# Kernel tuning notes

Hardware: AMD Instinct MI355X
Metric: run time of the kernel (lower is better)

The kernel has to match this reference:

```python
import jax, jax.numpy as jnp
import numpy as np

N, E, R, H = 20000, 320000, 8, 4
KG, CC = 128, 4
IN, HID, OUT = 256, 256, 256  # in_channels = KG + 128 (GCN out)
HO1, HO2 = HID // H, OUT // H  # per-head out channels
SLOPE_ACT = 0.01   # nn.LeakyReLU default
SLOPE_ATT = 0.2    # RGATConv negative_slope default


def gcn_conv(x, W, b, src, dst):
    """PyG GCNConv: add self loops, symmetric norm, x@W, scatter-sum, +bias."""
    n = x.shape[0]
    loop = jnp.arange(n, dtype=src.dtype)
    s = jnp.concatenate([src, loop])
    d = jnp.concatenate([dst, loop])
    deg = jnp.zeros((n,), x.dtype).at[d].add(1.0)
    dis = jnp.where(deg > 0, jax.lax.rsqrt(jnp.maximum(deg, 1.0)), 0.0)
    norm = dis[s] * dis[d]                        # [E+N]
    h = x @ W                                     # [n, out]
    out = jax.ops.segment_sum(norm[:, None] * h[s], d, num_segments=n)
    return out + b


def rgat_conv(x, W, q, k, b, src, dst, edge_type, heads, oc):
    """PyG RGATConv (additive-self-attention, across-relation, dim=1, concat)."""
    n = x.shape[0]
    xw = jnp.einsum('ni,rio->rno', x, W)          # [R, n, heads*oc]
    out_i = xw[edge_type, dst]                    # [E, heads*oc]
    out_j = xw[edge_type, src]                    # [E, heads*oc]
    qi = out_i @ q                                # [E, heads]
    kj = out_j @ k                                # [E, heads]
    alpha = jax.nn.leaky_relu(qi + kj, SLOPE_ATT)
    # softmax over incoming edges per destination node (across-relation)
    amax = jax.ops.segment_max(alpha, dst, num_segments=n)[dst]
    ex = jnp.exp(alpha - amax)
    denom = jax.ops.segment_sum(ex, dst, num_segments=n)[dst]
    alpha = ex / denom                            # [E, heads]
    e = src.shape[0]
    msg = (alpha[:, :, None] * out_j.reshape(e, heads, oc)).reshape(e, heads * oc)
    out = jax.ops.segment_sum(msg, dst, num_segments=n) + b
    return out, alpha


def setup_inputs() -> dict:
    key = jax.random.key(0)
    ks = jax.random.split(key, 16)
    d = {}
    d['kg_emb'] = jax.random.normal(ks[0], (N, KG), jnp.float32)
    d['ccle0'] = jax.random.normal(ks[1], (N, CC), jnp.float32)
    d['gcn_w1'] = jax.random.normal(ks[2], (CC, 32), jnp.float32) / np.float32(np.sqrt(CC))
    d['gcn_b1'] = jnp.zeros((32,), jnp.float32)
    d['gcn_w2'] = jax.random.normal(ks[3], (32, 128), jnp.float32) / np.float32(np.sqrt(32))
    d['gcn_b2'] = jnp.zeros((128,), jnp.float32)
    d['rgat1_w'] = jax.random.normal(ks[4], (R, IN, HID), jnp.float32) / np.float32(np.sqrt(IN))
    d['rgat1_q'] = jax.random.normal(ks[5], (HID, H), jnp.float32) / np.float32(np.sqrt(HID))
    d['rgat1_k'] = jax.random.normal(ks[6], (HID, H), jnp.float32) / np.float32(np.sqrt(HID))
    d['rgat1_b'] = jnp.zeros((HID,), jnp.float32)
    d['rgat2_w'] = jax.random.normal(ks[7], (R, HID, OUT), jnp.float32) / np.float32(np.sqrt(HID))
    d['rgat2_q'] = jax.random.normal(ks[8], (OUT, H), jnp.float32) / np.float32(np.sqrt(OUT))
    d['rgat2_k'] = jax.random.normal(ks[9], (OUT, H), jnp.float32) / np.float32(np.sqrt(OUT))
    d['rgat2_b'] = jnp.zeros((OUT,), jnp.float32)
    d['lin_w'] = jax.random.normal(ks[10], (IN, OUT), jnp.float32) / np.float32(np.sqrt(IN))
    d['lin_b'] = jnp.zeros((OUT,), jnp.float32)
    d['edge_index'] = jax.random.randint(ks[11], (2, E), 0, N, jnp.int32)
    d['edge_type'] = jax.random.randint(ks[12], (E,), 0, R, jnp.int32)
    return d


def reference(kg_emb, ccle0, gcn_w1, gcn_b1, gcn_w2, gcn_b2,
              rgat1_w, rgat1_q, rgat1_k, rgat1_b,
              rgat2_w, rgat2_q, rgat2_k, rgat2_b,
              lin_w, lin_b, edge_index, edge_type):
    src, dst = edge_index[0], edge_index[1]
    # ccle_layer: GCN(4->32) -> LeakyReLU -> GCN(32->128)
    c = gcn_conv(ccle0, gcn_w1, gcn_b1, src, dst)
    c = jax.nn.leaky_relu(c, SLOPE_ACT)
    c = gcn_conv(c, gcn_w2, gcn_b2, src, dst)
    # node_id = arange(N): concat(kg_emb, ccle_out)
    x0 = jnp.concatenate([kg_emb, c], axis=1)     # [N, IN]
    h, a1 = rgat_conv(x0, rgat1_w, rgat1_q, rgat1_k, rgat1_b,
                      src, dst, edge_type, H, HO1)
    h = jax.nn.leaky_relu(h, SLOPE_ACT)           # dropout p=0 -> identity
    h, a2 = rgat_conv(h, rgat2_w, rgat2_q, rgat2_k, rgat2_b,
                      src, dst, edge_type, H, HO2)
    out = h + (x0 @ lin_w + lin_b)                # residual through self.lin
    return out, a1, a2
```

## Files before the change

kernel.cpp:

```cpp
#include <hip/hip_runtime.h>
#include <cstdint>

static constexpr int N = 20000;
static constexpr int E = 320000;
static constexpr int R = 8;
static constexpr int H = 4;
static constexpr int C = 256;

using short8 = __attribute__((ext_vector_type(8))) short;
using f32x4  = __attribute__((ext_vector_type(4))) float;
using us4    = __attribute__((ext_vector_type(4))) unsigned short;

__device__ __forceinline__ float lrelu(float x, float s) { return x >= 0.f ? x : s * x; }
__device__ __forceinline__ unsigned short f2bf(float f) {
    unsigned u = __float_as_uint(f);
    unsigned r = (u + 0x7FFFu + ((u >> 16) & 1u)) >> 16;
    return (unsigned short)r;
}
__device__ __forceinline__ float bf2f(unsigned short s) {
    return __uint_as_float(((unsigned)s) << 16);
}

__device__ __forceinline__ void gl2l16(const unsigned short* g, unsigned short* l) {
    __builtin_amdgcn_global_load_lds(
        (const __attribute__((address_space(1))) unsigned int*)g,
        (__attribute__((address_space(3))) unsigned int*)l, 16, 0, 0);
}

__global__ void k_zero_int(int* p, int n) {
    int i = blockIdx.x * blockDim.x + threadIdx.x;
    if (i < n) p[i] = 0;
}

__global__ void k_count(const int* __restrict__ ei, int* __restrict__ cnt) {
    int e = blockIdx.x * blockDim.x + threadIdx.x;
    if (e < E) atomicAdd(&cnt[ei[E + e]], 1);
}

__global__ __launch_bounds__(1024) void k_scan(const int* __restrict__ cnt,
                                               int* __restrict__ rowptr,
                                               int* __restrict__ cursor,
                                               float* __restrict__ dis) {
    __shared__ int part[1024];
    const int CH = (N + 1023) / 1024;
    int t = threadIdx.x;
    int base = t * CH;
    int sum = 0;
    for (int j = 0; j < CH; ++j) {
        int idx = base + j;
        if (idx < N) sum += cnt[idx];
    }
    part[t] = sum;
    __syncthreads();
    for (int off = 1; off < 1024; off <<= 1) {
        int v = 0;
        if (t >= off) v = part[t - off];
        __syncthreads();
        if (t >= off) part[t] += v;
        __syncthreads();
    }
    int run = part[t] - sum;
    for (int j = 0; j < CH; ++j) {
        int idx = base + j;
        if (idx < N) {
            int cv = cnt[idx];
            rowptr[idx] = run;
            cursor[idx] = run;
            dis[idx] = rsqrtf((float)cv + 1.0f);
            run += cv;
        }
    }
    if (t == 1023) rowptr[N] = part[1023];
}

__global__ void k_scatter(const int* __restrict__ ei, const int* __restrict__ et,
                          int* __restrict__ cursor, int* __restrict__ csr_se,
                          int* __restrict__ csr_eid) {
    int e = blockIdx.x * blockDim.x + threadIdx.x;
    if (e >= E) return;
    int d = ei[E + e];
    int pos = atomicAdd(&cursor[d], 1);
    csr_se[pos] = (et[e] << 16) | ei[e];
    csr_eid[pos] = e;
}

__global__ void k_h1(const float* __restrict__ x, const float* __restrict__ W,
                     float* __restrict__ h) {
    int idx = blockIdx.x * blockDim.x + threadIdx.x;
    if (idx >= N * 32) return;
    int n = idx >> 5, f = idx & 31;
    const float* xr = x + n * 4;
    float acc = 0.f;
#pragma unroll
    for (int c = 0; c < 4; ++c) acc += xr[c] * W[c * 32 + f];
    h[idx] = acc;
}

__global__ void k_agg32(const int* __restrict__ rowptr, const int* __restrict__ csr_se,
                        const float* __restrict__ dis, const float* __restrict__ h,
                        const float* __restrict__ b, float* __restrict__ c) {
    int idx = blockIdx.x * blockDim.x + threadIdx.x;
    if (idx >= N * 32) return;
    int d = idx >> 5, f = idx & 31;
    int beg = rowptr[d], end = rowptr[d + 1];
    float acc = 0.f;
    for (int i = beg; i < end; ++i) {
        int s = csr_se[i] & 0xFFFF;
        acc += dis[s] * h[s * 32 + f];
    }
    float dd = dis[d];
    c[idx] = dd * acc + dd * dd * h[idx] + b[f];
}

__global__ void k_h2kg(const float* __restrict__ c1, const float* __restrict__ W,
                       const float* __restrict__ kg, unsigned short* __restrict__ h,
                       float* __restrict__ x0, unsigned short* __restrict__ xb0) {
    int idx = blockIdx.x * blockDim.x + threadIdx.x;
    if (idx >= N * 128) return;
    int n = idx >> 7, f = idx & 127;
    const float* cr = c1 + n * 32;
    float acc = 0.f;
    for (int c = 0; c < 32; ++c) acc += lrelu(cr[c], 0.01f) * W[c * 128 + f];
    h[idx] = f2bf(acc);
    float v = kg[idx];
    x0[n * 256 + f] = v;
    xb0[n * 256 + f] = f2bf(v);
}

__global__ void k_agg128(const int* __restrict__ rowptr, const int* __restrict__ csr_se,
                         const float* __restrict__ dis,
                         const unsigned short* __restrict__ h,
                         const float* __restrict__ b, float* __restrict__ x0,
                         unsigned short* __restrict__ xb0) {
    int idx = blockIdx.x * blockDim.x + threadIdx.x;
    if (idx >= N * 128) return;
    int d = idx >> 7, f = idx & 127;
    int beg = rowptr[d], end = rowptr[d + 1];
    float acc = 0.f;
    int i = beg;
    for (; i + 2 <= end; i += 2) {
        int s0 = csr_se[i] & 0xFFFF;
        int s1 = csr_se[i + 1] & 0xFFFF;
        float d0 = dis[s0], d1 = dis[s1];
        float v0 = bf2f(h[s0 * 128 + f]), v1 = bf2f(h[s1 * 128 + f]);
        acc += d0 * v0 + d1 * v1;
    }
    if (i < end) {
        int s = csr_se[i] & 0xFFFF;
        acc += dis[s] * bf2f(h[s * 128 + f]);
    }
    float dd = dis[d];
    float v = dd * acc + dd * dd * bf2f(h[d * 128 + f]) + b[f];
    x0[d * 256 + 128 + f] = v;
    xb0[d * 256 + 128 + f] = f2bf(v);
}

__global__ __launch_bounds__(256) void k_wqkb(const float* __restrict__ W,
                                              const float* __restrict__ q,
                                              const float* __restrict__ kmat,
                                              unsigned short* __restrict__ wqkb) {
    int w = (blockIdx.x * blockDim.x + threadIdx.x) >> 6;
    int lane = threadIdx.x & 63;
    int r = w >> 8, i = w & 255;
    const float* wr = W + ((size_t)(r * 256 + i)) * 256;
    float4 a = *(const float4*)(wr + lane * 4);
    float aq0 = 0.f, aq1 = 0.f, aq2 = 0.f, aq3 = 0.f;
    float ak0 = 0.f, ak1 = 0.f, ak2 = 0.f, ak3 = 0.f;
    int o = lane * 4;
    const float av[4] = {a.x, a.y, a.z, a.w};
#pragma unroll
    for (int j = 0; j < 4; ++j) {
        float4 qv = *(const float4*)(q + (o + j) * 4);
        float4 kv = *(const float4*)(kmat + (o + j) * 4);
        aq0 += av[j] * qv.x; aq1 += av[j] * qv.y;
        aq2 += av[j] * qv.z; aq3 += av[j] * qv.w;
        ak0 += av[j] * kv.x; ak1 += av[j] * kv.y;
        ak2 += av[j] * kv.z; ak3 += av[j] * kv.w;
    }
#pragma unroll
    for (int d = 1; d < 64; d <<= 1) {
        aq0 += __shfl_xor(aq0, d); aq1 += __shfl_xor(aq1, d);
        aq2 += __shfl_xor(aq2, d); aq3 += __shfl_xor(aq3, d);
        ak0 += __shfl_xor(ak0, d); ak1 += __shfl_xor(ak1, d);
        ak2 += __shfl_xor(ak2, d); ak3 += __shfl_xor(ak3, d);
    }
    if (lane == 0) {
        int nq = r * 4, nk = 32 + r * 4;
        wqkb[(nq + 0) * 256 + i] = f2bf(aq0);
        wqkb[(nq + 1) * 256 + i] = f2bf(aq1);
        wqkb[(nq + 2) * 256 + i] = f2bf(aq2);
        wqkb[(nq + 3) * 256 + i] = f2bf(aq3);
        wqkb[(nk + 0) * 256 + i] = f2bf(ak0);
        wqkb[(nk + 1) * 256 + i] = f2bf(ak1);
        wqkb[(nk + 2) * 256 + i] = f2bf(ak2);
        wqkb[(nk + 3) * 256 + i] = f2bf(ak3);
    }
}

#define QP 264
__global__ __launch_bounds__(256) void k_qnkn_mfma(
    const unsigned short* __restrict__ xb, const unsigned short* __restrict__ wqkb,
    float* __restrict__ qn, float* __restrict__ kn)
{
    __shared__ unsigned short Ws[64 * QP];
    int t = threadIdx.x;
    {
        int r = t >> 2, off = (t & 3) * 64;
#pragma unroll
        for (int i = 0; i < 8; ++i)
            *(uint4*)(&Ws[r * QP + off + i * 8]) =
                *(const uint4*)(wqkb + r * 256 + off + i * 8);
    }
    __syncthreads();
    int wave = t >> 6, lane = t & 63;
    int lrow = lane & 15, kq = lane >> 4;
    int mw = blockIdx.x * 64 + wave * 16;
    int gm = mw + lrow;
    int gmc = gm < N ? gm : N - 1;

    f32x4 acc[4];
#pragma unroll
    for (int j = 0; j < 4; ++j) acc[j] = (f32x4){0.f, 0.f, 0.f, 0.f};

    for (int k0 = 0; k0 < 8; ++k0) {
        short8 af = *(const short8*)(xb + (size_t)gmc * 256 + k0 * 32 + kq * 8);
#pragma unroll
        for (int j = 0; j < 4; ++j) {
            short8 bf4 = *(const short8*)(&Ws[(j * 16 + lrow) * QP + k0 * 32 + kq * 8]);
            acc[j] = __builtin_amdgcn_mfma_f32_16x16x32_bf16(bf4, af, acc[j], 0, 0, 0);
        }
    }
    if (gm < N) {
#pragma unroll
        for (int j = 0; j < 4; ++j) {
            int colb = j * 16 + kq * 4;
            float4 v = {acc[j][0], acc[j][1], acc[j][2], acc[j][3]};
            if (colb < 32) *(float4*)(qn + (size_t)gm * 32 + colb) = v;
            else           *(float4*)(kn + (size_t)gm * 32 + (colb - 32)) = v;
        }
    }
}

__global__ void k_soft(const int* __restrict__ rowptr, const int* __restrict__ csr_se,
                       const int* __restrict__ csr_eid,
                       const float* __restrict__ qn, const float* __restrict__ kn,
                       float* __restrict__ alpha_csr, float* __restrict__ aout) {
    int wid = (blockIdx.x * blockDim.x + threadIdx.x) >> 6;
    int lane = threadIdx.x & 63;
    if (wid >= N) return;
    int d = wid;
    int beg = rowptr[d], end = rowptr[d + 1];
    if (beg >= end) return;
    int slot = lane >> 2, h = lane & 3;
    int nc = (end - beg + 15) >> 4;
    const float* qrow = qn + d * 32;

    auto rawv = [&](int i) {
        int se = csr_se[i];
        int tt = se >> 16, s = se & 0xFFFF;
        return lrelu(qrow[tt * 4 + h] + kn[s * 32 + tt * 4 + h], 0.2f);
    };

    float av[4];
    float m = -1e30f;
    for (int c = 0; c < nc; ++c) {
        int i = beg + c * 16 + slot;
        float v = (i < end) ? rawv(i) : -1e30f;
        if (c < 4) av[c] = v;
        m = fmaxf(m, v);
    }
    m = fmaxf(m, __shfl_xor(m, 4));
    m = fmaxf(m, __shfl_xor(m, 8));
    m = fmaxf(m, __shfl_xor(m, 16));
    m = fmaxf(m, __shfl_xor(m, 32));

    float sum = 0.f;
    for (int c = 0; c < nc; ++c) {
        int i = beg + c * 16 + slot;
        float ex = 0.f;
        if (i < end) {
            float v = (c < 4) ? av[c] : rawv(i);
            ex = expf(v - m);
        }
        if (c < 4) av[c] = ex;
        sum += ex;
    }
    sum += __shfl_xor(sum, 4);
    sum += __shfl_xor(sum, 8);
    sum += __shfl_xor(sum, 16);
    sum += __shfl_xor(sum, 32);
    float inv = 1.f / sum;

    for (int c = 0; c < nc; ++c) {
        int i = beg + c * 16 + slot;
        if (i < end) {
            float ex = (c < 4) ? av[c] : expf(rawv(i) - m);
            float a = ex * inv;
            alpha_csr[i * 4 + h] = a;
            aout[csr_eid[i] * 4 + h] = a;
        }
    }
}

#define WTP 72
__global__ __launch_bounds__(256) void k_wconv_t(const float* __restrict__ W,
                                                 unsigned short* __restrict__ Wt) {
    int bid = blockIdx.x;
    int z = bid >> 4;
    int tile = bid & 15;
    int k0 = (tile >> 2) * 64, n0 = (tile & 3) * 64;
    __shared__ unsigned short T[64 * WTP];
    int t = threadIdx.x;
    const float* Wz = W + ((size_t)z << 16);
    int r = t >> 4;
    int cs = (t & 15) * 4;
#pragma unroll
    for (int rr = 0; rr < 4; ++rr) {
        int k = r + rr * 16;
        float4 v = *(const float4*)(Wz + (size_t)(k0 + k) * 256 + n0 + cs);
        T[(cs + 0) * WTP + k] = f2bf(v.x);
        T[(cs + 1) * WTP + k] = f2bf(v.y);
        T[(cs + 2) * WTP + k] = f2bf(v.z);
        T[(cs + 3) * WTP + k] = f2bf(v.w);
    }
    __syncthreads();
    int n = t >> 2, ck = (t & 3) * 16;
    unsigned short* dst = Wt + ((size_t)z << 16) + (size_t)(n0 + n) * 256 + k0 + ck;
    const unsigned short* srcp = T + n * WTP + ck;
    *(uint4*)(dst) = *(const uint4*)(srcp);
    *(uint4*)(dst + 8) = *(const uint4*)(srcp + 8);
}

#define TM 128
#define TN 128
__global__ __launch_bounds__(256) void gemm_mfma4(
    const unsigned short* __restrict__ A, const unsigned short* __restrict__ Bt,
    unsigned short* __restrict__ Cbf, float* __restrict__ Cf,
    const float* __restrict__ bias, const float* __restrict__ bias2,
    int M, int NZ, int NT, int MT, int zlin)
{
    __shared__ unsigned short As[128 * 32];
    __shared__ unsigned short Bs[128 * 32];

    int bi = blockIdx.x;
    int cx = bi & 7;
    int g = bi >> 3;
    int per = NZ * NT;
    int mh = g / per;
    int j  = g % per;
    int mt = mh * 8 + cx;
    if (mt >= MT) return;
    int z  = j % NZ;
    int nb = j / NZ;
    int m0 = mt * TM;
    int n0 = nb * TN;

    const unsigned short* Bz = Bt + ((size_t)z << 16);
    int t = threadIdx.x;
    int wave = t >> 6, lane = t & 63;
    int wr = wave >> 1, wc = wave & 1;
    int lrow = lane & 15, kq = lane >> 4;

    int sr0 = (wave * 2 + 0) * 16 + (lane >> 2);
    int sr1 = (wave * 2 + 1) * 16 + (lane >> 2);
    int sc = (((lane & 3) ^ ((lane >> 3) & 3))) * 8;
    int gm0 = m0 + sr0; if (gm0 >= M) gm0 = M - 1;
    int gm1 = m0 + sr1; if (gm1 >= M) gm1 = M - 1;
    const unsigned short* gA0 = A + (size_t)gm0 * 256 + sc;
    const unsigned short* gA1 = A + (size_t)gm1 * 256 + sc;
    const unsigned short* gB0 = Bz + (size_t)(n0 + sr0) * 256 + sc;
    const unsigned short* gB1 = Bz + (size_t)(n0 + sr1) * 256 + sc;
    unsigned short* lA0 = &As[(wave * 2 + 0) * 512];
    unsigned short* lA1 = &As[(wave * 2 + 1) * 512];
    unsigned short* lB0 = &Bs[(wave * 2 + 0) * 512];
    unsigned short* lB1 = &Bs[(wave * 2 + 1) * 512];

    int rg = (kq ^ ((lrow >> 1) & 3)) * 8;

    f32x4 acc[4][4];
#pragma unroll
    for (int i = 0; i < 4; ++i)
#pragma unroll
        for (int jj = 0; jj < 4; ++jj) acc[i][jj] = (f32x4){0.f, 0.f, 0.f, 0.f};

    for (int k0 = 0; k0 < 256; k0 += 32) {
        gl2l16(gA0 + k0, lA0);
        gl2l16(gA1 + k0, lA1);
        gl2l16(gB0 + k0, lB0);
        gl2l16(gB1 + k0, lB1);
        __syncthreads();
        short8 af[4], bf4[4];
#pragma unroll
        for (int i = 0; i < 4; ++i)
            af[i] = *(const short8*)(&As[(wr * 64 + i * 16 + lrow) * 32 + rg]);
#pragma unroll
        for (int jj = 0; jj < 4; ++jj)
            bf4[jj] = *(const short8*)(&Bs[(wc * 64 + jj * 16 + lrow) * 32 + rg]);
#pragma unroll
        for (int i = 0; i < 4; ++i)
#pragma unroll
            for (int jj = 0; jj < 4; ++jj)
                acc[i][jj] = __builtin_amdgcn_mfma_f32_16x16x32_bf16(bf4[jj], af[i],
                                                                     acc[i][jj], 0, 0, 0);
        __syncthreads();
    }
    if (z == zlin) {
#pragma unroll
        for (int i = 0; i < 4; ++i) {
            int gm = m0 + wr * 64 + i * 16 + lrow;
            if (gm >= M) continue;
#pragma unroll
            for (int jj = 0; jj < 4; ++jj) {
                int gnb = n0 + wc * 64 + jj * 16 + kq * 4;
                float4 b1 = *(const float4*)(bias + gnb);
                float4 b2 = *(const float4*)(bias2 + gnb);
                float4 v = {acc[i][jj][0] + b1.x + b2.x,
                            acc[i][jj][1] + b1.y + b2.y,
                            acc[i][jj][2] + b1.z + b2.z,
                            acc[i][jj][3] + b1.w + b2.w};
                *(float4*)(Cf + (size_t)gm * 256 + gnb) = v;
            }
        }
    } else {
#pragma unroll
        for (int i = 0; i < 4; ++i) {
            int gm = m0 + wr * 64 + i * 16 + lrow;
            if (gm >= M) continue;
#pragma unroll
            for (int jj = 0; jj < 4; ++jj) {
                int gnb = n0 + wc * 64 + jj * 16 + kq * 4;
                us4 v = {f2bf(acc[i][jj][0]), f2bf(acc[i][jj][1]),
                         f2bf(acc[i][jj][2]), f2bf(acc[i][jj][3])};
                *(us4*)(Cbf + ((size_t)z * M + gm) * 256 + gnb) = v;
            }
        }
    }
}

__global__ __launch_bounds__(256) void k_msg_gather(
    const int* __restrict__ rowptr, const int* __restrict__ csr_se,
    const float* __restrict__ alpha_csr, const unsigned short* __restrict__ xw,
    const float* __restrict__ bias, float* __restrict__ out,
    unsigned short* __restrict__ xbout, int r0, int r1, int first, int act) {
    __shared__ float Pf[2][256];
    int tid = threadIdx.x;
    int wave = tid >> 6, lane = tid & 63;
    int nslot = wave >> 1, p = wave & 1;
    int node = blockIdx.x * 2 + nslot;
    int hsel = lane >> 4;
    float ax = 0.f, ay = 0.f, az = 0.f, aw = 0.f;

    auto edge = [&](int i) {
        int se = csr_se[i];
        int tt = se >> 16;
        if (tt >= r0 && tt < r1) {
            int s = se & 0xFFFF;
            float a = alpha_csr[i * 4 + hsel];
            uint2 pv = *(const uint2*)(xw + ((size_t)(tt - r0) * N + s) * 256 + lane * 4);
            ax += a * __uint_as_float(pv.x << 16);
            ay += a * __uint_as_float(pv.x & 0xFFFF0000u);
            az += a * __uint_as_float(pv.y << 16);
            aw += a * __uint_as_float(pv.y & 0xFFFF0000u);
        }
    };

    if (node < N) {
        int beg = rowptr[node], end = rowptr[node + 1];
        int i = beg + p;
        for (; i + 2 < end; i += 4) { edge(i); edge(i + 2); }
        if (i < end) edge(i);
    }
    if (p == 1) {
        float4 v = {ax, ay, az, aw};
        *(float4*)(&Pf[nslot][lane * 4]) = v;
    }
    __syncthreads();
    if (p == 0 && node < N) {
        float4 q = *(const float4*)(&Pf[nslot][lane * 4]);
        ax += q.x; ay += q.y; az += q.z; aw += q.w;
        float* o = out + (size_t)node * 256 + lane * 4;
        float vx, vy, vz, vw;
        if (first) {
            const float4 b = ((const float4*)bias)[lane];
            vx = ax + b.x; vy = ay + b.y; vz = az + b.z; vw = aw + b.w;
        } else {
            vx = o[0] + ax; vy = o[1] + ay; vz = o[2] + az; vw = o[3] + aw;
        }
        if (act) {
            vx = lrelu(vx, 0.01f); vy = lrelu(vy, 0.01f);
            vz = lrelu(vz, 0.01f); vw = lrelu(vw, 0.01f);
            unsigned short* xo = xbout + (size_t)node * 256 + lane * 4;
            xo[0] = f2bf(vx); xo[1] = f2bf(vy); xo[2] = f2bf(vz); xo[3] = f2bf(vw);
        }
        o[0] = vx; o[1] = vy; o[2] = vz; o[3] = vw;
    }
}

extern "C" void kernel_launch(void* const* d_in, const int* in_sizes, int n_in,
                              void* d_out, int out_size, void* d_ws, size_t ws_size,
                              hipStream_t stream) {
    const float* kg   = (const float*)d_in[0];
    const float* cc0  = (const float*)d_in[1];
    const float* gw1  = (const float*)d_in[2];
    const float* gb1  = (const float*)d_in[3];
    const float* gw2  = (const float*)d_in[4];
    const float* gb2  = (const float*)d_in[5];
    const float* r1w  = (const float*)d_in[6];
    const float* r1q  = (const float*)d_in[7];
    const float* r1k  = (const float*)d_in[8];
    const float* r1b  = (const float*)d_in[9];
    const float* r2w  = (const float*)d_in[10];
    const float* r2q  = (const float*)d_in[11];
    const float* r2k  = (const float*)d_in[12];
    const float* r2b  = (const float*)d_in[13];
    const float* linw = (const float*)d_in[14];
    const float* linb = (const float*)d_in[15];
    const int*   ei   = (const int*)d_in[16];
    const int*   et   = (const int*)d_in[17];

    float* out = (float*)d_out;
    float* a1  = out + (size_t)N * C;
    float* a2  = a1 + (size_t)E * H;

    float* ws = (float*)d_ws;
    size_t off = 0;
    float* dis  = ws + off; off += N;
    float* h1   = ws + off; off += (size_t)N * 32;
    float* c1   = ws + off; off += (size_t)N * 32;
    unsigned short* h2b = (unsigned short*)(ws + off); off += (size_t)N * 64;
    float* x0   = ws + off; off += (size_t)N * C;
    float* hmid = ws + off; off += (size_t)N * C;
    float* qn   = ws + off; off += (size_t)N * R * H;
    float* kn   = ws + off; off += (size_t)N * R * H;
    int* cnt     = (int*)(ws + off); off += N;
    int* rowptr  = (int*)(ws + off); off += N + 1;
    int* cursor  = (int*)(ws + off); off += N;
    int* csr_se  = (int*)(ws + off); off += E;
    int* csr_eid = (int*)(ws + off); off += E;
    float* alpha = ws + off; off += (size_t)E * H;
    unsigned short* xb0 = (unsigned short*)(ws + off); off += (size_t)N * 128;
    unsigned short* xb1 = (unsigned short*)(ws + off); off += (size_t)N * 128;
    unsigned short* wt  = (unsigned short*)(ws + off); off += (size_t)(R + 1) * 32768;
    unsigned short* wtl = wt + ((size_t)R << 16);
    unsigned short* wqkb = (unsigned short*)(ws + off); off += 8192;
    unsigned short* xwb = (unsigned short*)(ws + off);

    size_t fixedB = off * 4;
    int K = R;
    if (ws_size > fixedB) {
        size_t kmax = (ws_size - fixedB) / ((size_t)N * C * 2);
        if (kmax < (size_t)K) K = (int)kmax;
    } else {
        K = 1;
    }
    if (K < 1) K = 1;

    const int B = 256;
    auto cdiv = [](long a, long b) { return (int)((a + b - 1) / b); };
    const int MT = cdiv(N, TM);
    const int NT = C / TN;

    k_zero_int<<<cdiv(N, B), B, 0, stream>>>(cnt, N);
    k_count<<<cdiv(E, B), B, 0, stream>>>(ei, cnt);
    k_scan<<<1, 1024, 0, stream>>>(cnt, rowptr, cursor, dis);
    k_scatter<<<cdiv(E, B), B, 0, stream>>>(ei, et, cursor, csr_se, csr_eid);

    k_h1<<<cdiv((long)N * 32, B), B, 0, stream>>>(cc0, gw1, h1);
    k_agg32<<<cdiv((long)N * 32, B), B, 0, stream>>>(rowptr, csr_se, dis, h1, gb1, c1);
    k_h2kg<<<cdiv((long)N * 128, B), B, 0, stream>>>(c1, gw2, kg, h2b, x0, xb0);
    k_agg128<<<cdiv((long)N * 128, B), B, 0, stream>>>(rowptr, csr_se, dis, h2b,
                                                       gb2, x0, xb0);

    auto rgat = [&](unsigned short* xb, const float* W,
                    const float* q, const float* kk, const float* b,
                    float* obuf, unsigned short* xbout, float* aout,
                    int first, int act, int lin, float* linout,
                    const float* lb1, const float* lb2) {
        k_wqkb<<<512, 256, 0, stream>>>(W, q, kk, wqkb);
        k_qnkn_mfma<<<cdiv(N, 64), B, 0, stream>>>(xb, wqkb, qn, kn);
        k_soft<<<cdiv((long)N * 64, B), B, 0, stream>>>(rowptr, csr_se, csr_eid,
                                                        qn, kn, alpha, aout);
        k_wconv_t<<<R * 16, 256, 0, stream>>>(W, wt);
        for (int r0 = 0; r0 < R; r0 += K) {
            int kc = (R - r0) < K ? (R - r0) : K;
            int addlin = (lin && (r0 + kc == R)) ? 1 : 0;
            int nz = kc + addlin;
            int zl = addlin ? kc : -1;
            int gx = 8 * nz * NT * cdiv(MT, 8);
            gemm_mfma4<<<gx, 256, 0, stream>>>(xb, wt + ((size_t)r0 << 16), xwb,
                                               linout, lb1, lb2,
                                               N, nz, NT, MT, zl);
            int last = (r0 + kc >= R) ? 1 : 0;
            k_msg_gather<<<cdiv(N, 2), 256, 0, stream>>>(
                rowptr, csr_se, alpha, xwb, b, obuf, xbout, r0, r0 + kc,
                (first && r0 == 0) ? 1 : 0, act && last);
        }
    };

    k_wconv_t<<<16, 256, 0, stream>>>(linw, wtl);

    rgat(xb0, r1w, r1q, r1k, r1b, hmid, xb1, a1, 1, 1,
         1, out, linb, r2b);

    rgat(xb1, r2w, r2q, r2k, r2b, out, nullptr, a2, 0, 0,
         0, nullptr, nullptr, nullptr);
}
```

Baseline: 525.3 us.

## Double-buffer LDS tiles in MFMA GEMM with async global-to-LDS prefetch

Converts the bf16 MFMA GEMM K-loop from a single LDS buffer to two buffers. The load for tile k+2 is issued while tile k is being computed, with explicit vmcnt waits and barriers replacing __syncthreads. The goal is to hide global-load latency behind MFMA work. It doubles LDS use per block, which may lower occupancy, and it relies on hand-written waitcnt ordering being correct.

```diff
diff --git a/kernel.cpp b/kernel.cpp
--- a/kernel.cpp
+++ b/kernel.cpp
@@ -339,8 +339,8 @@
     const float* __restrict__ bias, const float* __restrict__ bias2,
     int M, int NZ, int NT, int MT, int zlin)
 {
-    __shared__ unsigned short As[128 * 32];
-    __shared__ unsigned short Bs[128 * 32];
+    __shared__ unsigned short As[2][128 * 32];
+    __shared__ unsigned short Bs[2][128 * 32];
 
     int bi = blockIdx.x;
     int cx = bi & 7;
@@ -370,10 +370,14 @@
     const unsigned short* gA1 = A + (size_t)gm1 * 256 + sc;
     const unsigned short* gB0 = Bz + (size_t)(n0 + sr0) * 256 + sc;
     const unsigned short* gB1 = Bz + (size_t)(n0 + sr1) * 256 + sc;
-    unsigned short* lA0 = &As[(wave * 2 + 0) * 512];
-    unsigned short* lA1 = &As[(wave * 2 + 1) * 512];
-    unsigned short* lB0 = &Bs[(wave * 2 + 0) * 512];
-    unsigned short* lB1 = &Bs[(wave * 2 + 1) * 512];
+
+    auto stage = [&](int b, int kt) {
+        int ko = kt * 32;
+        gl2l16(gA0 + ko, &As[b][(wave * 2 + 0) * 512]);
+        gl2l16(gA1 + ko, &As[b][(wave * 2 + 1) * 512]);
+        gl2l16(gB0 + ko, &Bs[b][(wave * 2 + 0) * 512]);
+        gl2l16(gB1 + ko, &Bs[b][(wave * 2 + 1) * 512]);
+    };
 
     int rg = (kq ^ ((lrow >> 1) & 3)) * 8;
 
@@ -383,27 +387,38 @@
 #pragma unroll
         for (int jj = 0; jj < 4; ++jj) acc[i][jj] = (f32x4){0.f, 0.f, 0.f, 0.f};
 
-    for (int k0 = 0; k0 < 256; k0 += 32) {
-        gl2l16(gA0 + k0, lA0);
-        gl2l16(gA1 + k0, lA1);
-        gl2l16(gB0 + k0, lB0);
-        gl2l16(gB1 + k0, lB1);
-        __syncthreads();
+    stage(0, 0);
+    stage(1, 1);
+
+    int cur = 0;
+#pragma unroll 1
+    for (int step = 0; step < 8; ++step) {
+        if (step < 7) asm volatile("s_waitcnt vmcnt(4)" ::: "memory");
+        else          asm volatile("s_waitcnt vmcnt(0)" ::: "memory");
+        __builtin_amdgcn_s_barrier();
+        __builtin_amdgcn_sched_barrier(0);
+
         short8 af[4], bf4[4];
 #pragma unroll
         for (int i = 0; i < 4; ++i)
-            af[i] = *(const short8*)(&As[(wr * 64 + i * 16 + lrow) * 32 + rg]);
+            af[i] = *(const short8*)(&As[cur][(wr * 64 + i * 16 + lrow) * 32 + rg]);
 #pragma unroll
         for (int jj = 0; jj < 4; ++jj)
-            bf4[jj] = *(const short8*)(&Bs[(wc * 64 + jj * 16 + lrow) * 32 + rg]);
+            bf4[jj] = *(const short8*)(&Bs[cur][(wc * 64 + jj * 16 + lrow) * 32 + rg]);
 #pragma unroll
         for (int i = 0; i < 4; ++i)
 #pragma unroll
             for (int jj = 0; jj < 4; ++jj)
                 acc[i][jj] = __builtin_amdgcn_mfma_f32_16x16x32_bf16(bf4[jj], af[i],
                                                                      acc[i][jj], 0, 0, 0);
-        __syncthreads();
-    }
+        __builtin_amdgcn_sched_barrier(0);
+        asm volatile("s_waitcnt lgkmcnt(0)" ::: "memory");
+        __builtin_amdgcn_s_barrier();
+        __builtin_amdgcn_sched_barrier(0);
+        if (step < 6) stage(cur, step + 2);
+        cur ^= 1;
+    }
+
     if (z == zlin) {
 #pragma unroll
         for (int i = 0; i < 4; ++i) {
```

Measured after the change: 524.6 us. Within noise of the previous version (-0.1%).
